# Kernel tuning notes

Hardware: AMD Instinct MI355X
Metric: run time of the kernel (lower is better)

Reference implementation:

```python
import jax, jax.numpy as jnp
import numpy as np

WS = 8  # window_size
EPS = 1e-5  # BatchNorm eps


def setup_inputs() -> dict:
    key = jax.random.key(0)
    ks = jax.random.split(key, 11)
    c = 64
    return {
        "x": jax.random.normal(ks[0], (4, c, 256, 256), dtype=jnp.float32),
        "w_in": jax.random.normal(ks[1], (c, c), dtype=jnp.float32) * 0.05,
        "b_in": jax.random.normal(ks[2], (c,), dtype=jnp.float32) * 0.05,
        "bn_gamma": jax.random.uniform(ks[3], (c,), dtype=jnp.float32),
        "bn_beta": jax.random.normal(ks[4], (c,), dtype=jnp.float32) * 0.05,
        "bn_mean": jax.random.normal(ks[5], (c,), dtype=jnp.float32) * 0.05,
        "bn_var": jax.random.uniform(ks[6], (c,), dtype=jnp.float32),
        "w_mask": jax.random.normal(ks[7], (c, c), dtype=jnp.float32) * 0.05,
        "b_mask": jax.random.normal(ks[8], (c,), dtype=jnp.float32) * 0.05,
        "w_out": jax.random.normal(ks[9], (c, c), dtype=jnp.float32) * 0.05,
        "b_out": jax.random.normal(ks[10], (c,), dtype=jnp.float32) * 0.05,
    }


def reference(x, w_in, b_in, bn_gamma, bn_beta, bn_mean, bn_var,
              w_mask, b_mask, w_out, b_out):
    ws = WS
    b, c, h, w = x.shape  # shifts == 0 -> no roll

    # project_inp: 1x1 conv + BatchNorm2d (inference mode, running stats)
    x = jnp.einsum('bchw,oc->bohw', x, w_in) + b_in[None, :, None, None]
    inv = bn_gamma / jnp.sqrt(bn_var + EPS)
    x = (x - bn_mean[None, :, None, None]) * inv[None, :, None, None] \
        + bn_beta[None, :, None, None]

    # seq_refl_win_pad(back=False): pad right/bottom by ws, then copy the
    # preceding ws rows into the bottom pad, then the preceding ws cols
    # (including the new bottom rows) into the right pad.
    x_pad = jnp.concatenate([x, x[:, :, -ws:, :]], axis=2)      # [b,c,h+ws,w]
    x_pad = jnp.concatenate([x_pad, x_pad[:, :, :, -ws:]], axis=3)  # [b,c,h+ws,w+ws]

    hh, ww = h // ws, w // ws
    # mask = Conv2d(kernel=1, stride=2) on the 2ws x 2ws windows ->
    # equivalent to sampling even offsets inside each window, then a 1x1 linear.
    row = (jnp.arange(hh) * ws)[:, None] + jnp.arange(0, 2 * ws, 2)[None, :]  # [hh, ws]
    col = (jnp.arange(ww) * ws)[:, None] + jnp.arange(0, 2 * ws, 2)[None, :]  # [ww, ws]
    g = x_pad[:, :, row, :]        # [b, c, hh, ws_h, w+ws]
    g = g[:, :, :, :, col]         # [b, c, hh, ws_h, ww, ws_w]
    # torch's double unfold yields window dims ordered (W-window, H-window),
    # and q flattens in that (Wwin, Hwin) order -> match exactly.
    g = jnp.transpose(g, (0, 2, 4, 5, 3, 1))        # [b, hh, ww, ws_w, ws_h, c]
    q = g.reshape(b * hh * ww, ws * ws, c)
    q = q @ w_mask.T + b_mask                       # 1x1 conv as per-pixel linear

    # v: non-overlapping ws x ws windows of x, flattened H-major (dh dw)
    v = x.reshape(b, c, hh, ws, ww, ws)
    v = jnp.transpose(v, (0, 2, 4, 3, 5, 1)).reshape(b * hh * ww, ws * ws, c)

    atn = jax.nn.softmax(q @ jnp.swapaxes(q, -1, -2), axis=-1)  # [bn, ws^2, ws^2]
    y = atn @ v                                                  # [bn, ws^2, c]

    # reassemble: '(b h w) (dh dw) c -> b c (h dh) (w dw)'
    y = y.reshape(b, hh, ww, ws, ws, c)
    y = jnp.transpose(y, (0, 5, 1, 3, 2, 4)).reshape(b, c, h, w)

    # project_out: 1x1 conv
    y = jnp.einsum('bchw,oc->bohw', y, w_out) + b_out[None, :, None, None]
    return y
```

## Files before the change

kernel.cpp:

```cpp
#include <hip/hip_runtime.h>

typedef unsigned short ushort_t;
typedef unsigned int uint_t;
typedef __attribute__((ext_vector_type(8))) short short8v;
typedef __attribute__((ext_vector_type(4))) float f32x4;

__device__ __forceinline__ float bf2f(ushort_t u) {
    union { uint_t u; float f; } v; v.u = (uint_t)u << 16; return v.f;
}
__device__ __forceinline__ ushort_t f2bf(float f) {
    union { float f; uint_t u; } v; v.f = f;
    uint_t u = v.u;
    return (ushort_t)((u + 0x7fffu + ((u >> 16) & 1u)) >> 16);
}

#define MFMA(A,B,C) __builtin_amdgcn_mfma_f32_16x16x32_bf16(A, B, C, 0, 0, 0)

__device__ __forceinline__ void split8(float4 f0, float4 f1, short8v& h8, short8v& l8) {
    float v[8] = {f0.x, f0.y, f0.z, f0.w, f1.x, f1.y, f1.z, f1.w};
    union { short8v v; ushort_t s[8]; } H, L;
    #pragma unroll
    for (int e = 0; e < 8; ++e) {
        ushort_t h = f2bf(v[e]);
        H.s[e] = h;
        L.s[e] = f2bf(v[e] - bf2f(h));
    }
    h8 = H.v; l8 = L.v;
}

__global__ __launch_bounds__(256, 4) void k1_pwbn_mfma(
    const float* __restrict__ x, const float* __restrict__ w_in, const float* __restrict__ b_in,
    const float* __restrict__ gamma, const float* __restrict__ beta,
    const float* __restrict__ mean, const float* __restrict__ var,
    ushort_t* __restrict__ xbn)
{
    __shared__ short xsh[64][72];
    __shared__ short xsl[64][72];
    __shared__ short wfh[64][72];
    __shared__ short wfl[64][72];
    __shared__ float bef[64];

    int tid = threadIdx.x;
    int b   = blockIdx.x >> 10;
    int hw0 = (blockIdx.x & 1023) << 6;
    const float* xb = x + ((size_t)b << 22);

    #pragma unroll
    for (int u = 0; u < 2; ++u) {
        int idx = u * 256 + tid;
        int cp = idx >> 4, pq = idx & 15;
        int c0 = cp * 2, p0 = pq * 4;
        float4 fa = *(const float4*)(xb + (size_t)c0 * 65536 + hw0 + p0);
        float4 fb = *(const float4*)(xb + (size_t)(c0 + 1) * 65536 + hw0 + p0);
        float va[4] = {fa.x, fa.y, fa.z, fa.w};
        float vb[4] = {fb.x, fb.y, fb.z, fb.w};
        #pragma unroll
        for (int e = 0; e < 4; ++e) {
            ushort_t h0 = f2bf(va[e]), h1 = f2bf(vb[e]);
            ushort_t l0 = f2bf(va[e] - bf2f(h0)), l1 = f2bf(vb[e] - bf2f(h1));
            *(uint_t*)&xsh[p0 + e][c0] = (uint_t)h0 | ((uint_t)h1 << 16);
            *(uint_t*)&xsl[p0 + e][c0] = (uint_t)l0 | ((uint_t)l1 << 16);
        }
    }
    #pragma unroll
    for (int v = 0; v < 2; ++v) {
        int idx = v * 256 + tid;
        int o = idx >> 3, c0 = (idx & 7) * 8;
        float sc = gamma[o] * rsqrtf(var[o] + 1e-5f);
        float4 fa = *(const float4*)(w_in + o * 64 + c0);
        float4 fb = *(const float4*)(w_in + o * 64 + c0 + 4);
        float vv[8] = {fa.x, fa.y, fa.z, fa.w, fb.x, fb.y, fb.z, fb.w};
        union { int4 q; ushort_t s[8]; } ph, pl;
        #pragma unroll
        for (int e = 0; e < 8; ++e) {
            float wv = vv[e] * sc;
            ushort_t h = f2bf(wv);
            ph.s[e] = h;
            pl.s[e] = f2bf(wv - bf2f(h));
        }
        *(int4*)&wfh[o][c0] = ph.q;
        *(int4*)&wfl[o][c0] = pl.q;
    }
    if (tid < 64) {
        float inv = gamma[tid] * rsqrtf(var[tid] + 1e-5f);
        bef[tid] = (b_in[tid] - mean[tid]) * inv + beta[tid];
    }
    __syncthreads();

    int w = tid >> 6, l = tid & 63;
    int half = l >> 4, lr = l & 15;
    int k0 = half * 8;

    short8v bh[2], bl[2];
    #pragma unroll
    for (int kc = 0; kc < 2; ++kc) {
        bh[kc] = *(short8v*)&xsh[16 * w + lr][k0 + 32 * kc];
        bl[kc] = *(short8v*)&xsl[16 * w + lr][k0 + 32 * kc];
    }
    short8v ah[4][2], al[4][2];
    #pragma unroll
    for (int ot = 0; ot < 4; ++ot)
        #pragma unroll
        for (int kc = 0; kc < 2; ++kc) {
            ah[ot][kc] = *(short8v*)&wfh[16 * ot + lr][k0 + 32 * kc];
            al[ot][kc] = *(short8v*)&wfl[16 * ot + lr][k0 + 32 * kc];
        }

    ushort_t* xp = xbn + ((size_t)(b * 65536 + hw0 + 16 * w + lr) << 6);
    #pragma unroll
    for (int ot = 0; ot < 4; ++ot) {
        f32x4 acc = {0.f, 0.f, 0.f, 0.f};
        #pragma unroll
        for (int kc = 0; kc < 2; ++kc) {
            acc = MFMA(ah[ot][kc], bh[kc], acc);
            acc = MFMA(ah[ot][kc], bl[kc], acc);
            acc = MFMA(al[ot][kc], bh[kc], acc);
        }
        int o0 = 16 * ot + 4 * half;
        float4 bq = *(const float4*)&bef[o0];
        float bqs[4] = {bq.x, bq.y, bq.z, bq.w};
        ushort_t hs[4];
        #pragma unroll
        for (int rr = 0; rr < 4; ++rr) hs[rr] = f2bf(acc[rr] + bqs[rr]);
        *(uint2*)(xp + o0) = make_uint2((uint_t)hs[0] | ((uint_t)hs[1] << 16),
                                        (uint_t)hs[2] | ((uint_t)hs[3] << 16));
    }
}

#define K2_A   0
#define K2_B   9216
#define K2_C   18432
#define K2_D   27648
#define K2_E   36864
#define K2_RS  53248
#define K2_TOT 53504

__global__ __launch_bounds__(256, 3) void k2_attn_v3(
    const ushort_t* __restrict__ xbn,
    const float* __restrict__ w_mask, const float* __restrict__ b_mask,
    const float* __restrict__ w_out,  const float* __restrict__ b_out,
    float* __restrict__ out)
{
    __shared__ char smem[K2_TOT];
    short* gb   = (short*)(smem + K2_A);
    short* vb   = (short*)(smem + K2_B);
    short* qhb  = (short*)(smem + K2_C);
    short* qlb  = (short*)(smem + K2_D);
    float* Sb   = (float*)(smem + K2_E);
    short* vwt  = (short*)(smem + K2_A);
    short* pt   = (short*)(smem + K2_B);
    float* outt = (float*)(smem + K2_E);
    float* rsv  = (float*)(smem + K2_RS);

    int tid = threadIdx.x;
    int wid = blockIdx.x;
    int b = wid >> 10, i = (wid >> 5) & 31, j = wid & 31;
    const ushort_t* xb = xbn + ((size_t)b << 22);

    {
        int t = tid >> 2, seg = tid & 3;
        int r = t & 7, s = t >> 3;
        int pr = i * 8 + 2 * r; if (pr >= 256) pr -= 8;
        int pc = j * 8 + 2 * s; if (pc >= 256) pc -= 8;
        const ushort_t* src = xb + (((size_t)((pr << 8) | pc)) << 6) + seg * 16;
        *(int4*)(gb + t * 72 + seg * 16)     = *(const int4*)src;
        *(int4*)(gb + t * 72 + seg * 16 + 8) = *(const int4*)(src + 8);
        int vr = i * 8 + (t >> 3), vc = j * 8 + (t & 7);
        const ushort_t* vsrc = xb + (((size_t)((vr << 8) | vc)) << 6) + seg * 16;
        *(int4*)(vb + t * 72 + seg * 16)     = *(const int4*)vsrc;
        *(int4*)(vb + t * 72 + seg * 16 + 8) = *(const int4*)(vsrc + 8);
    }
    __syncthreads();

    int w = tid >> 6, l = tid & 63;
    int half = l >> 4, lr = l & 15;
    int mrow = (16 * w + lr) * 72;
    int kc0 = half * 8, kc1 = 32 + half * 8;
    int swz = lr & 7;

    {
        const float* wmp = w_mask + (16 * w + lr) * 64;
        short8v amh0, aml0, amh1, aml1;
        split8(*(const float4*)(wmp + kc0), *(const float4*)(wmp + kc0 + 4), amh0, aml0);
        split8(*(const float4*)(wmp + kc1), *(const float4*)(wmp + kc1 + 4), amh1, aml1);
        float4 bm = *(const float4*)(b_mask + 16 * w + half * 4);
        float bmv[4] = {bm.x, bm.y, bm.z, bm.w};
        #pragma unroll
        for (int n = 0; n < 4; ++n) {
            int nrow = (16 * n + lr) * 72;
            short8v bg0 = *(short8v*)(gb + nrow + kc0);
            short8v bg1 = *(short8v*)(gb + nrow + kc1);
            f32x4 acc = {0.f, 0.f, 0.f, 0.f};
            acc = MFMA(amh0, bg0, acc);
            acc = MFMA(amh1, bg1, acc);
            acc = MFMA(aml0, bg0, acc);
            acc = MFMA(aml1, bg1, acc);
            ushort_t hs[4], ls[4];
            #pragma unroll
            for (int rr = 0; rr < 4; ++rr) {
                float qv = acc[rr] + bmv[rr];
                hs[rr] = f2bf(qv);
                ls[rr] = f2bf(qv - bf2f(hs[rr]));
            }
            int qoff = (16 * n + lr) * 72 + 16 * w + half * 4;
            *(uint2*)(qhb + qoff) = make_uint2((uint_t)hs[0] | ((uint_t)hs[1] << 16),
                                               (uint_t)hs[2] | ((uint_t)hs[3] << 16));
            *(uint2*)(qlb + qoff) = make_uint2((uint_t)ls[0] | ((uint_t)ls[1] << 16),
                                               (uint_t)ls[2] | ((uint_t)ls[3] << 16));
        }
    }
    __syncthreads();

    {
        short8v av0 = *(short8v*)(vb + mrow + kc0);
        short8v av1 = *(short8v*)(vb + mrow + kc1);
        #pragma unroll
        for (int n = 0; n < 4; ++n) {
            const float* wop = w_out + (16 * n + lr) * 64;
            short8v bh0, bl0, bh1, bl1;
            split8(*(const float4*)(wop + kc0), *(const float4*)(wop + kc0 + 4), bh0, bl0);
            split8(*(const float4*)(wop + kc1), *(const float4*)(wop + kc1 + 4), bh1, bl1);
            f32x4 acc = {0.f, 0.f, 0.f, 0.f};
            acc = MFMA(av0, bh0, acc);
            acc = MFMA(av1, bh1, acc);
            acc = MFMA(av0, bl0, acc);
            acc = MFMA(av1, bl1, acc);
            ushort_t hs[4];
            #pragma unroll
            for (int rr = 0; rr < 4; ++rr) hs[rr] = f2bf(acc[rr]);
            int voff = (16 * n + lr) * 72 + 16 * w + half * 4;
            *(uint2*)(vwt + voff) = make_uint2((uint_t)hs[0] | ((uint_t)hs[1] << 16),
                                               (uint_t)hs[2] | ((uint_t)hs[3] << 16));
        }
    }
    {
        short8v ah0 = *(short8v*)(qhb + mrow + kc0);
        short8v ah1 = *(short8v*)(qhb + mrow + kc1);
        short8v al0 = *(short8v*)(qlb + mrow + kc0);
        short8v al1 = *(short8v*)(qlb + mrow + kc1);
        #pragma unroll
        for (int n = 0; n < 4; ++n) {
            int nrow = (16 * n + lr) * 72;
            short8v bh0 = *(short8v*)(qhb + nrow + kc0);
            short8v bh1 = *(short8v*)(qhb + nrow + kc1);
            short8v bl0 = *(short8v*)(qlb + nrow + kc0);
            short8v bl1 = *(short8v*)(qlb + nrow + kc1);
            f32x4 acc = {0.f, 0.f, 0.f, 0.f};
            acc = MFMA(ah0, bh0, acc);
            acc = MFMA(ah1, bh1, acc);
            acc = MFMA(ah0, bl0, acc);
            acc = MFMA(ah1, bl1, acc);
            acc = MFMA(al0, bh0, acc);
            acc = MFMA(al1, bh1, acc);
            int srow = 16 * n + lr;
            int c4s = (4 * w + half) ^ swz;
            *(f32x4*)(Sb + srow * 64 + c4s * 4) = acc;
        }
    }
    __syncthreads();

    {
        int row = tid >> 2, p = tid & 3;
        int rsw = row & 7;
        const float* srow = Sb + row * 64;
        f32x4 s4[4];
        #pragma unroll
        for (int qq = 0; qq < 4; ++qq)
            s4[qq] = *(const f32x4*)(srow + (p * 4 + qq) * 4);
        float m = -1e30f;
        #pragma unroll
        for (int qq = 0; qq < 4; ++qq)
            m = fmaxf(m, fmaxf(fmaxf(s4[qq][0], s4[qq][1]), fmaxf(s4[qq][2], s4[qq][3])));
        m = fmaxf(m, __shfl_xor(m, 1));
        m = fmaxf(m, __shfl_xor(m, 2));
        float ssum = 0.f;
        #pragma unroll
        for (int qq = 0; qq < 4; ++qq) {
            int ucol4 = (p * 4 + qq) ^ rsw;
            ushort_t hs[4];
            #pragma unroll
            for (int e = 0; e < 4; ++e) {
                ushort_t h = f2bf(__expf(s4[qq][e] - m));
                ssum += bf2f(h);
                hs[e] = h;
            }
            *(uint2*)(pt + row * 72 + ucol4 * 4) =
                make_uint2((uint_t)hs[0] | ((uint_t)hs[1] << 16),
                           (uint_t)hs[2] | ((uint_t)hs[3] << 16));
        }
        ssum += __shfl_xor(ssum, 1);
        ssum += __shfl_xor(ssum, 2);
        if (p == 0) rsv[row] = 1.0f / ssum;
    }
    __syncthreads();

    {
        short8v ap0 = *(short8v*)(pt + mrow + kc0);
        short8v ap1 = *(short8v*)(pt + mrow + kc1);
        float4 rv = *(const float4*)(rsv + 16 * w + half * 4);
        float rvv[4] = {rv.x, rv.y, rv.z, rv.w};
        #pragma unroll
        for (int n = 0; n < 4; ++n) {
            int nrow = (16 * n + lr) * 72;
            short8v bv0 = *(short8v*)(vwt + nrow + kc0);
            short8v bv1 = *(short8v*)(vwt + nrow + kc1);
            f32x4 acc = {0.f, 0.f, 0.f, 0.f};
            acc = MFMA(ap0, bv0, acc);
            acc = MFMA(ap1, bv1, acc);
            int orow = 16 * n + lr;
            float bo = b_out[orow];
            int c4s = (4 * w + half) ^ swz;
            f32x4 wv = {acc[0] * rvv[0] + bo, acc[1] * rvv[1] + bo,
                        acc[2] * rvv[2] + bo, acc[3] * rvv[3] + bo};
            *(f32x4*)(outt + orow * 64 + c4s * 4) = wv;
        }
    }
    __syncthreads();

    {
        float* ob = out + ((size_t)b << 22);
        int base = (i * 8) * 256 + j * 8;
        for (int pp = 0; pp < 16; ++pp) {
            int e = pp * 256 + tid;
            int o = e >> 6, t = e & 63;
            float val = outt[o * 64 + (((t >> 2) ^ (o & 7)) << 2) + (t & 3)];
            ob[((size_t)o << 16) + base + ((t >> 3) << 8) + (t & 7)] = val;
        }
    }
}

extern "C" void kernel_launch(void* const* d_in, const int* in_sizes, int n_in,
                              void* d_out, int out_size, void* d_ws, size_t ws_size,
                              hipStream_t stream) {
    const float* x      = (const float*)d_in[0];
    const float* w_in   = (const float*)d_in[1];
    const float* b_in   = (const float*)d_in[2];
    const float* gamma  = (const float*)d_in[3];
    const float* beta   = (const float*)d_in[4];
    const float* mean   = (const float*)d_in[5];
    const float* var    = (const float*)d_in[6];
    const float* w_mask = (const float*)d_in[7];
    const float* b_mask = (const float*)d_in[8];
    const float* w_out  = (const float*)d_in[9];
    const float* b_out  = (const float*)d_in[10];
    float* out = (float*)d_out;
    ushort_t* xbn = (ushort_t*)d_ws;

    hipLaunchKernelGGL(k1_pwbn_mfma, dim3(4096), dim3(256), 0, stream,
                       x, w_in, b_in, gamma, beta, mean, var, xbn);
    hipLaunchKernelGGL(k2_attn_v3, dim3(4096), dim3(256), 0, stream,
                       xbn, w_mask, b_mask, w_out, b_out, out);
}
```

Measured before the change: 196.9 us.

## Keep attention scores in registers and shrink shared memory for higher occupancy

The attention kernel no longer stages the 64x64 fp32 score matrix in shared memory. Scores stay in MFMA accumulator registers, and the row max and row sum are reduced through small cross-wave buffers. The V-projection and PV GEMMs are re-tiled so each wave owns one slice of output channels, which lets each wave load and split its w_out rows once. w_mask and w_out loads are also hoisted ahead of the first barrier. Shared memory drops from about 53KB to 38KB so launch bounds can allow 4 blocks per CU, at the cost of an extra barrier-separated reduction step and more register pressure.

```diff
diff --git a/kernel.cpp b/kernel.cpp
--- a/kernel.cpp
+++ b/kernel.cpp
@@ -127,35 +127,47 @@
     }
 }
 
-#define K2_A   0
-#define K2_B   9216
-#define K2_C   18432
-#define K2_D   27648
-#define K2_E   36864
-#define K2_RS  53248
-#define K2_TOT 53504
-
-__global__ __launch_bounds__(256, 3) void k2_attn_v3(
+#define K4_G    0
+#define K4_V    9216
+#define K4_QH   18432
+#define K4_QL   27648
+#define K4_RED  36864
+#define K4_RED2 37888
+#define K4_TOT  38912
+
+__global__ __launch_bounds__(256, 4) void k2_attn_v4(
     const ushort_t* __restrict__ xbn,
     const float* __restrict__ w_mask, const float* __restrict__ b_mask,
     const float* __restrict__ w_out,  const float* __restrict__ b_out,
     float* __restrict__ out)
 {
-    __shared__ char smem[K2_TOT];
-    short* gb   = (short*)(smem + K2_A);
-    short* vb   = (short*)(smem + K2_B);
-    short* qhb  = (short*)(smem + K2_C);
-    short* qlb  = (short*)(smem + K2_D);
-    float* Sb   = (float*)(smem + K2_E);
-    short* vwt  = (short*)(smem + K2_A);
-    short* pt   = (short*)(smem + K2_B);
-    float* outt = (float*)(smem + K2_E);
-    float* rsv  = (float*)(smem + K2_RS);
+    __shared__ char smem[K4_TOT];
+    short* gb   = (short*)(smem + K4_G);
+    short* vb   = (short*)(smem + K4_V);
+    short* qhb  = (short*)(smem + K4_QH);
+    short* qlb  = (short*)(smem + K4_QL);
+    short* vwt  = (short*)(smem + K4_G);
+    short* pt   = (short*)(smem + K4_V);
+    float* outt = (float*)(smem + K4_QH);
+    float* red  = (float*)(smem + K4_RED);
+    float* red2 = (float*)(smem + K4_RED2);
 
     int tid = threadIdx.x;
     int wid = blockIdx.x;
     int b = wid >> 10, i = (wid >> 5) & 31, j = wid & 31;
     const ushort_t* xb = xbn + ((size_t)b << 22);
+
+    int w = tid >> 6, l = tid & 63;
+    int half = l >> 4, lr = l & 15;
+    int mrow = (16 * w + lr) * 72;
+    int kc0 = half * 8, kc1 = 32 + half * 8;
+
+    const float* wmp = w_mask + (16 * w + lr) * 64;
+    const float* wop = w_out  + (16 * w + lr) * 64;
+    float4 wmA = *(const float4*)(wmp + kc0), wmB = *(const float4*)(wmp + kc0 + 4);
+    float4 wmC = *(const float4*)(wmp + kc1), wmD = *(const float4*)(wmp + kc1 + 4);
+    float4 woA = *(const float4*)(wop + kc0), woB = *(const float4*)(wop + kc0 + 4);
+    float4 woC = *(const float4*)(wop + kc1), woD = *(const float4*)(wop + kc1 + 4);
 
     {
         int t = tid >> 2, seg = tid & 3;
@@ -172,17 +184,10 @@
     }
     __syncthreads();
 
-    int w = tid >> 6, l = tid & 63;
-    int half = l >> 4, lr = l & 15;
-    int mrow = (16 * w + lr) * 72;
-    int kc0 = half * 8, kc1 = 32 + half * 8;
-    int swz = lr & 7;
-
-    {
-        const float* wmp = w_mask + (16 * w + lr) * 64;
+    {
         short8v amh0, aml0, amh1, aml1;
-        split8(*(const float4*)(wmp + kc0), *(const float4*)(wmp + kc0 + 4), amh0, aml0);
-        split8(*(const float4*)(wmp + kc1), *(const float4*)(wmp + kc1 + 4), amh1, aml1);
+        split8(wmA, wmB, amh0, aml0);
+        split8(wmC, wmD, amh1, aml1);
         float4 bm = *(const float4*)(b_mask + 16 * w + half * 4);
         float bmv[4] = {bm.x, bm.y, bm.z, bm.w};
         #pragma unroll
@@ -212,14 +217,14 @@
     __syncthreads();
 
     {
-        short8v av0 = *(short8v*)(vb + mrow + kc0);
-        short8v av1 = *(short8v*)(vb + mrow + kc1);
-        #pragma unroll
-        for (int n = 0; n < 4; ++n) {
-            const float* wop = w_out + (16 * n + lr) * 64;
-            short8v bh0, bl0, bh1, bl1;
-            split8(*(const float4*)(wop + kc0), *(const float4*)(wop + kc0 + 4), bh0, bl0);
-            split8(*(const float4*)(wop + kc1), *(const float4*)(wop + kc1 + 4), bh1, bl1);
+        short8v bh0, bl0, bh1, bl1;
+        split8(woA, woB, bh0, bl0);
+        split8(woC, woD, bh1, bl1);
+        #pragma unroll
+        for (int mm = 0; mm < 4; ++mm) {
+            int arow = (16 * mm + lr) * 72;
+            short8v av0 = *(short8v*)(vb + arow + kc0);
+            short8v av1 = *(short8v*)(vb + arow + kc1);
             f32x4 acc = {0.f, 0.f, 0.f, 0.f};
             acc = MFMA(av0, bh0, acc);
             acc = MFMA(av1, bh1, acc);
@@ -228,11 +233,12 @@
             ushort_t hs[4];
             #pragma unroll
             for (int rr = 0; rr < 4; ++rr) hs[rr] = f2bf(acc[rr]);
-            int voff = (16 * n + lr) * 72 + 16 * w + half * 4;
+            int voff = (16 * w + lr) * 72 + 16 * mm + 4 * half;
             *(uint2*)(vwt + voff) = make_uint2((uint_t)hs[0] | ((uint_t)hs[1] << 16),
                                                (uint_t)hs[2] | ((uint_t)hs[3] << 16));
         }
     }
+    f32x4 sreg[4];
     {
         short8v ah0 = *(short8v*)(qhb + mrow + kc0);
         short8v ah1 = *(short8v*)(qhb + mrow + kc1);
@@ -252,67 +258,65 @@
             acc = MFMA(ah1, bl1, acc);
             acc = MFMA(al0, bh0, acc);
             acc = MFMA(al1, bh1, acc);
-            int srow = 16 * n + lr;
-            int c4s = (4 * w + half) ^ swz;
-            *(f32x4*)(Sb + srow * 64 + c4s * 4) = acc;
-        }
-    }
-    __syncthreads();
-
-    {
-        int row = tid >> 2, p = tid & 3;
-        int rsw = row & 7;
-        const float* srow = Sb + row * 64;
-        f32x4 s4[4];
-        #pragma unroll
-        for (int qq = 0; qq < 4; ++qq)
-            s4[qq] = *(const f32x4*)(srow + (p * 4 + qq) * 4);
-        float m = -1e30f;
-        #pragma unroll
-        for (int qq = 0; qq < 4; ++qq)
-            m = fmaxf(m, fmaxf(fmaxf(s4[qq][0], s4[qq][1]), fmaxf(s4[qq][2], s4[qq][3])));
-        m = fmaxf(m, __shfl_xor(m, 1));
-        m = fmaxf(m, __shfl_xor(m, 2));
-        float ssum = 0.f;
-        #pragma unroll
-        for (int qq = 0; qq < 4; ++qq) {
-            int ucol4 = (p * 4 + qq) ^ rsw;
+            sreg[n] = acc;
+        }
+        #pragma unroll
+        for (int n = 0; n < 4; ++n) {
+            float pm = fmaxf(fmaxf(sreg[n][0], sreg[n][1]), fmaxf(sreg[n][2], sreg[n][3]));
+            pm = fmaxf(pm, __shfl_xor(pm, 16));
+            pm = fmaxf(pm, __shfl_xor(pm, 32));
+            if (half == 0) red[(16 * n + lr) * 4 + w] = pm;
+        }
+    }
+    __syncthreads();
+
+    {
+        #pragma unroll
+        for (int n = 0; n < 4; ++n) {
+            int t = 16 * n + lr;
+            float4 r4 = *(const float4*)&red[t * 4];
+            float m = fmaxf(fmaxf(r4.x, r4.y), fmaxf(r4.z, r4.w));
             ushort_t hs[4];
+            float ps = 0.f;
             #pragma unroll
-            for (int e = 0; e < 4; ++e) {
-                ushort_t h = f2bf(__expf(s4[qq][e] - m));
-                ssum += bf2f(h);
-                hs[e] = h;
+            for (int rr = 0; rr < 4; ++rr) {
+                ushort_t h = f2bf(__expf(sreg[n][rr] - m));
+                ps += bf2f(h);
+                hs[rr] = h;
             }
-            *(uint2*)(pt + row * 72 + ucol4 * 4) =
+            *(uint2*)(pt + t * 72 + 16 * w + 4 * half) =
                 make_uint2((uint_t)hs[0] | ((uint_t)hs[1] << 16),
                            (uint_t)hs[2] | ((uint_t)hs[3] << 16));
-        }
-        ssum += __shfl_xor(ssum, 1);
-        ssum += __shfl_xor(ssum, 2);
-        if (p == 0) rsv[row] = 1.0f / ssum;
-    }
-    __syncthreads();
-
-    {
-        short8v ap0 = *(short8v*)(pt + mrow + kc0);
-        short8v ap1 = *(short8v*)(pt + mrow + kc1);
-        float4 rv = *(const float4*)(rsv + 16 * w + half * 4);
-        float rvv[4] = {rv.x, rv.y, rv.z, rv.w};
-        #pragma unroll
-        for (int n = 0; n < 4; ++n) {
-            int nrow = (16 * n + lr) * 72;
-            short8v bv0 = *(short8v*)(vwt + nrow + kc0);
-            short8v bv1 = *(short8v*)(vwt + nrow + kc1);
+            ps += __shfl_xor(ps, 16);
+            ps += __shfl_xor(ps, 32);
+            if (half == 0) red2[t * 4 + w] = ps;
+        }
+    }
+    __syncthreads();
+
+    {
+        short8v bv0 = *(short8v*)(vwt + mrow + kc0);
+        short8v bv1 = *(short8v*)(vwt + mrow + kc1);
+        float bo = b_out[16 * w + lr];
+        int swz = lr & 7;
+        #pragma unroll
+        for (int mm = 0; mm < 4; ++mm) {
+            int arow = (16 * mm + lr) * 72;
+            short8v ap0 = *(short8v*)(pt + arow + kc0);
+            short8v ap1 = *(short8v*)(pt + arow + kc1);
             f32x4 acc = {0.f, 0.f, 0.f, 0.f};
             acc = MFMA(ap0, bv0, acc);
             acc = MFMA(ap1, bv1, acc);
-            int orow = 16 * n + lr;
-            float bo = b_out[orow];
-            int c4s = (4 * w + half) ^ swz;
-            f32x4 wv = {acc[0] * rvv[0] + bo, acc[1] * rvv[1] + bo,
-                        acc[2] * rvv[2] + bo, acc[3] * rvv[3] + bo};
-            *(f32x4*)(outt + orow * 64 + c4s * 4) = wv;
+            f32x4 wv;
+            #pragma unroll
+            for (int rr = 0; rr < 4; ++rr) {
+                int t = 16 * mm + 4 * half + rr;
+                float4 s4 = *(const float4*)&red2[t * 4];
+                float inv = 1.0f / (s4.x + s4.y + s4.z + s4.w);
+                wv[rr] = acc[rr] * inv + bo;
+            }
+            int c4s = (4 * mm + half) ^ swz;
+            *(f32x4*)(outt + (16 * w + lr) * 64 + c4s * 4) = wv;
         }
     }
     __syncthreads();
@@ -348,6 +352,6 @@
 
     hipLaunchKernelGGL(k1_pwbn_mfma, dim3(4096), dim3(256), 0, stream,
                        x, w_in, b_in, gamma, beta, mean, var, xbn);
-    hipLaunchKernelGGL(k2_attn_v3, dim3(4096), dim3(256), 0, stream,
+    hipLaunchKernelGGL(k2_attn_v4, dim3(4096), dim3(256), 0, stream,
                        xbn, w_mask, b_mask, w_out, b_out, out);
 }
```

After: 186.9 us. 1.05x faster.
